# Performance work log

Measured on AMD Instinct MI355X. Metric: run time of the kernel, lower is better.

The kernel has to match this reference:

```python
import jax, jax.numpy as jnp
import numpy as np

N, L, H, D = 2, 4096, 12, 64
HD = H * D

def setup_inputs() -> dict:
    key = jax.random.key(0)
    ks = jax.random.split(key, 5)
    s = 1.0 / np.sqrt(HD)  # keep projections well-scaled
    return {
        "x": jax.random.normal(ks[0], (N, L, HD), dtype=jnp.float32),
        "Wq": jax.random.normal(ks[1], (HD, HD), dtype=jnp.float32) * s,
        "bq": jnp.zeros((HD,), dtype=jnp.float32),
        "Wk": jax.random.normal(ks[2], (HD, HD), dtype=jnp.float32) * s,
        "bk": jnp.zeros((HD,), dtype=jnp.float32),
        "Wv": jax.random.normal(ks[3], (HD, HD), dtype=jnp.float32) * s,
        "bv": jnp.zeros((HD,), dtype=jnp.float32),
        "Wo": jax.random.normal(ks[4], (HD, HD), dtype=jnp.float32) * s,
        "bo": jnp.zeros((HD,), dtype=jnp.float32),
        "train": 0,
    }

def reference(x, Wq, bq, Wk, bk, Wv, bv, Wo, bo, train):
    n, l, hd = x.shape
    h, d = H, D
    # QKV projections (hk.Linear: x @ W + b), reshape to (n, l, h, d)
    q = (x @ Wq + bq).reshape(n, l, h, d)
    k = (x @ Wk + bk).reshape(n, l, h, d)
    v = (x @ Wv + bv).reshape(n, l, h, d)
    # scores: (n, q, k, h), scaled by sqrt(key_size)
    qkt = jnp.einsum('nqhd,nkhd->nqkh', q, k) / jnp.sqrt(jnp.float32(d))
    attn = jax.nn.softmax(qkt, axis=2)
    # eval mode: dropout_rate is 0.0, so dropout is identity
    o = jnp.einsum('nqkh,nkhd->nqhd', attn, v).reshape(n, l, hd)
    return o @ Wo + bo
```

## Files before the change

kernel.cpp:

```cpp
#include <hip/hip_runtime.h>

#define NN 2
#define LL 4096
#define HH 12
#define DD 64
#define HD_ 768
#define M_TOT (NN * LL)
#define KVSTRIDE 262144

typedef __bf16 bf16_t;
typedef _Float16 f16_t;
typedef __bf16 bf16x8 __attribute__((ext_vector_type(8)));
typedef __bf16 bf16x4 __attribute__((ext_vector_type(4)));
typedef _Float16 f16x2 __attribute__((ext_vector_type(2)));
typedef _Float16 f16x4 __attribute__((ext_vector_type(4)));
typedef _Float16 f16x8 __attribute__((ext_vector_type(8)));
typedef float floatx4 __attribute__((ext_vector_type(4)));
typedef float floatx16 __attribute__((ext_vector_type(16)));

#define QSCALE 0.1803368801111f

__device__ __forceinline__ void async_load16(const void* g, void* l) {
    __builtin_amdgcn_global_load_lds(
        (const __attribute__((address_space(1))) unsigned int*)(g),
        (__attribute__((address_space(3))) unsigned int*)(l),
        16, 0, 0);
}

__device__ __forceinline__ f16x2 pkrtz(float a, float b) {
    return __builtin_bit_cast(f16x2, __builtin_amdgcn_cvt_pkrtz(a, b));
}

__device__ __forceinline__ f16x4 shflx32(f16x4 v) {
    int2 iv = __builtin_bit_cast(int2, v);
    iv.x = __shfl_xor(iv.x, 32);
    iv.y = __shfl_xor(iv.y, 32);
    return __builtin_bit_cast(f16x4, iv);
}

__global__ void cvt_kernel(const float* __restrict__ src, bf16_t* __restrict__ dst, int n4) {
    int i = blockIdx.x * blockDim.x + threadIdx.x;
    if (i < n4) {
        const float4 v = ((const float4*)src)[i];
        bf16_t* d = dst + (size_t)i * 4;
        d[0] = (bf16_t)v.x; d[1] = (bf16_t)v.y; d[2] = (bf16_t)v.z; d[3] = (bf16_t)v.w;
    }
}

struct WtArgs { const float* W[4]; bf16_t* Wt[4]; };
__global__ void cvt_wt_kernel(WtArgs a) {
    const int z = blockIdx.z;
    int id = blockIdx.x * 256 + threadIdx.x;
    int k = id / HD_;
    int n = id % HD_;
    a.Wt[z][(size_t)n * HD_ + k] = (bf16_t)a.W[z][id];
}

__device__ __forceinline__ void gemm_tile128(
    const bf16_t* __restrict__ A, const bf16_t* __restrict__ Bt,
    bf16_t* As, bf16_t* Bs, int m0, int n0, floatx4 (&acc)[4][4])
{
    const int tid  = threadIdx.x;
    const int w    = tid >> 6, lane = tid & 63;
    const int quad = lane >> 4, l16 = lane & 15;
    const int wm = w >> 1, wn = w & 1;
    const int rsub = lane >> 3;
    const int csub = (lane & 7) * 8;

    const bf16_t* aBase = A + (size_t)(m0 + w * 32 + rsub) * HD_ + csub;
    const bf16_t* bBase = Bt + (size_t)(n0 + w * 32 + rsub) * HD_ + csub;

    for (int kt = 0; kt < HD_; kt += 64) {
        __syncthreads();
        for (int i = 0; i < 4; ++i) {
            const int ar = w * 32 + i * 8;
            async_load16(aBase + (size_t)i * 8 * HD_ + kt, As + ar * 64 + lane * 8);
            async_load16(bBase + (size_t)i * 8 * HD_ + kt, Bs + ar * 64 + lane * 8);
        }
        __syncthreads();
        for (int ks = 0; ks < 2; ++ks) {
            bf16x8 af[4], bf[4];
            for (int mi = 0; mi < 4; ++mi)
                af[mi] = *(const bf16x8*)&As[(wm * 64 + mi * 16 + l16) * 64 + ks * 32 + quad * 8];
            for (int ni = 0; ni < 4; ++ni)
                bf[ni] = *(const bf16x8*)&Bs[(wn * 64 + ni * 16 + l16) * 64 + ks * 32 + quad * 8];
            for (int mi = 0; mi < 4; ++mi)
                for (int ni = 0; ni < 4; ++ni)
                    acc[mi][ni] = __builtin_amdgcn_mfma_f32_16x16x32_bf16(
                        af[mi], bf[ni], acc[mi][ni], 0, 0, 0);
        }
    }
}

struct QKVArgs {
    const bf16_t* Bt[3];
    const float* bias[3];
    void* out[3];
};
__global__ __launch_bounds__(256) void gemm_qkv_kernel(const bf16_t* __restrict__ A, QKVArgs p)
{
    __shared__ __align__(16) bf16_t As[128 * 64];
    __shared__ __align__(16) bf16_t Bs[128 * 64];
    const int z = blockIdx.z;
    const int m0 = blockIdx.y * 128, n0 = blockIdx.x * 128;

    floatx4 acc[4][4] = {};
    gemm_tile128(A, p.Bt[z], As, Bs, m0, n0, acc);

    const int tid  = threadIdx.x;
    const int lane = tid & 63;
    const int quad = lane >> 4, l16 = lane & 15;
    const int w    = tid >> 6;
    const int wm = w >> 1, wn = w & 1;
    const float scale = (z == 0) ? QSCALE : 1.0f;
    const float* bias = p.bias[z];

    for (int ni = 0; ni < 4; ++ni) {
        const int col = n0 + wn * 64 + ni * 16 + l16;
        const float bv = bias[col];
        const int h = col >> 6, d = col & 63;
        for (int mi = 0; mi < 4; ++mi) {
            for (int r = 0; r < 4; ++r) {
                const int row = m0 + wm * 64 + mi * 16 + quad * 4 + r;
                const float val = (acc[mi][ni][r] + bv) * scale;
                const int nn = row >> 12, l = row & 4095;
                const size_t nhb = (size_t)(nn * HH + h) * KVSTRIDE;
                if (z == 0) {
                    ((bf16_t*)p.out[0])[(((size_t)nn * HH + h) * LL + l) * DD + d] = (bf16_t)val;
                } else if (z == 1) {
                    size_t idx = nhb + (size_t)((l >> 5) * 4 + (d >> 4)) * 512
                               + ((l & 31) + 32 * ((d >> 3) & 1)) * 8 + (d & 7);
                    ((bf16_t*)p.out[1])[idx] = (bf16_t)val;
                } else {
                    size_t idx = nhb + (size_t)(((l >> 6) * 2 + (d >> 5)) * 4 + ((l >> 4) & 3)) * 512
                               + ((d & 31) + 32 * ((l >> 3) & 1)) * 8 + (l & 7);
                    ((f16_t*)p.out[2])[idx] = (f16_t)val;
                }
            }
        }
    }
}

__global__ __launch_bounds__(256) void gemm_o_kernel(
    const bf16_t* __restrict__ A, const bf16_t* __restrict__ Bt,
    const float* __restrict__ bias, float* __restrict__ Cout)
{
    __shared__ __align__(16) bf16_t As[128 * 64];
    __shared__ __align__(16) bf16_t Bs[128 * 64];
    const int m0 = blockIdx.y * 128, n0 = blockIdx.x * 128;

    floatx4 acc[4][4] = {};
    gemm_tile128(A, Bt, As, Bs, m0, n0, acc);

    const int tid  = threadIdx.x;
    const int lane = tid & 63;
    const int quad = lane >> 4, l16 = lane & 15;
    const int w    = tid >> 6;
    const int wm = w >> 1, wn = w & 1;

    for (int ni = 0; ni < 4; ++ni) {
        const int col = n0 + wn * 64 + ni * 16 + l16;
        const float bv = bias[col];
        for (int mi = 0; mi < 4; ++mi)
            for (int r = 0; r < 4; ++r) {
                const int row = m0 + wm * 64 + mi * 16 + quad * 4 + r;
                Cout[(size_t)row * HD_ + col] = acc[mi][ni][r] + bv;
            }
    }
}

__global__ __launch_bounds__(256) void attn_kernel(
    const bf16_t* __restrict__ qg, const bf16_t* __restrict__ kf,
    const f16_t* __restrict__ vf, bf16_t* __restrict__ og)
{
    __shared__ union {
        struct {
            bf16_t Ks[8 * 512];
            f16_t  Vs[8 * 512];
        } s;
        bf16_t OT[128 * 72];
    } u;

    const int tid = threadIdx.x;
    const int w = tid >> 6, lane = tid & 63;
    const int l32 = lane & 31, hi = lane >> 5;
    const int qt0 = blockIdx.x * 128;
    const int nh = blockIdx.y;
    const int nIdx = nh / HH, hIdx = nh % HH;

    bf16x8 qfrag[4];
    {
        const bf16_t* qp = qg + ((size_t)nh * LL + qt0 + w * 32 + l32) * DD + hi * 8;
        for (int s = 0; s < 4; ++s) qfrag[s] = *(const bf16x8*)(qp + s * 16);
    }

    const bf16_t* ksrc = kf + (size_t)nh * KVSTRIDE + (2 * w) * 512 + lane * 8;
    const f16_t*  vsrc = vf + (size_t)nh * KVSTRIDE + (2 * w) * 512 + lane * 8;
    bf16_t* kdst0 = &u.s.Ks[(2 * w) * 512 + lane * 8];
    bf16_t* kdst1 = &u.s.Ks[(2 * w + 1) * 512 + lane * 8];
    f16_t*  vdst0 = &u.s.Vs[(2 * w) * 512 + lane * 8];
    f16_t*  vdst1 = &u.s.Vs[(2 * w + 1) * 512 + lane * 8];

    floatx16 oacc[2] = {};
    float rs = 0.f;

    for (int t = 0; t < LL / 64; ++t) {
        __syncthreads();
        async_load16(ksrc, kdst0);
        async_load16(ksrc + 512, kdst1);
        async_load16(vsrc, vdst0);
        async_load16(vsrc + 512, vdst1);
        ksrc += 4096; vsrc += 4096;
        __syncthreads();

        for (int kvb = 0; kvb < 2; ++kvb) {
            floatx16 sacc = {};
            for (int s = 0; s < 4; ++s) {
                bf16x8 ak = *(const bf16x8*)&u.s.Ks[(kvb * 4 + s) * 512 + lane * 8];
                sacc = __builtin_amdgcn_mfma_f32_32x32x16_bf16(ak, qfrag[s], sacc, 0, 0, 0);
            }
            for (int sub = 0; sub < 2; ++sub) {
                float p[8];
                for (int i = 0; i < 8; ++i) {
                    p[i] = __builtin_amdgcn_exp2f(sacc[sub * 8 + i]);
                    rs += p[i];
                }
                f16x2 l01 = pkrtz(p[0], p[1]), l23 = pkrtz(p[2], p[3]);
                f16x2 h45 = pkrtz(p[4], p[5]), h67 = pkrtz(p[6], p[7]);
                f16x4 Lo = __builtin_shufflevector(l01, l23, 0, 1, 2, 3);
                f16x4 Hh = __builtin_shufflevector(h45, h67, 0, 1, 2, 3);
                f16x4 swL = shflx32(Lo);
                f16x4 swH = shflx32(Hh);
                f16x4 a03 = hi ? swH : Lo;
                f16x4 a47 = hi ? Hh : swL;
                f16x8 pf = __builtin_shufflevector(a03, a47, 0, 1, 2, 3, 4, 5, 6, 7);
                const int kstep = kvb * 2 + sub;
                for (int db = 0; db < 2; ++db) {
                    f16x8 av = *(const f16x8*)&u.s.Vs[(db * 4 + kstep) * 512 + lane * 8];
                    oacc[db] = __builtin_amdgcn_mfma_f32_32x32x16_f16(av, pf, oacc[db], 0, 0, 0);
                }
            }
        }
    }

    rs += __shfl_xor(rs, 32);
    const float rinv = __builtin_amdgcn_rcpf(rs);

    __syncthreads();
    for (int db = 0; db < 2; ++db)
        for (int g = 0; g < 4; ++g) {
            bf16x4 o4;
            for (int r = 0; r < 4; ++r)
                o4[r] = (bf16_t)(oacc[db][g * 4 + r] * rinv);
            *(bf16x4*)&u.OT[(w * 32 + l32) * 72 + db * 32 + hi * 4 + g * 8] = o4;
        }
    __syncthreads();

    const int q = tid >> 1, hf = tid & 1;
    const bf16_t* src = &u.OT[q * 72 + hf * 32];
    bf16x8 r0 = *(const bf16x8*)(src + 0);
    bf16x8 r1 = *(const bf16x8*)(src + 8);
    bf16x8 r2 = *(const bf16x8*)(src + 16);
    bf16x8 r3 = *(const bf16x8*)(src + 24);
    bf16_t* dst = og + ((size_t)nIdx * LL + qt0 + q) * HD_ + hIdx * 64 + hf * 32;
    *(bf16x8*)(dst + 0)  = r0;
    *(bf16x8*)(dst + 8)  = r1;
    *(bf16x8*)(dst + 16) = r2;
    *(bf16x8*)(dst + 24) = r3;
}

extern "C" void kernel_launch(void* const* d_in, const int* in_sizes, int n_in,
                              void* d_out, int out_size, void* d_ws, size_t ws_size,
                              hipStream_t stream) {
    const float* x  = (const float*)d_in[0];
    const float* Wq = (const float*)d_in[1];
    const float* bq = (const float*)d_in[2];
    const float* Wk = (const float*)d_in[3];
    const float* bk = (const float*)d_in[4];
    const float* Wv = (const float*)d_in[5];
    const float* bv = (const float*)d_in[6];
    const float* Wo = (const float*)d_in[7];
    const float* bo = (const float*)d_in[8];

    char* ws = (char*)d_ws;
    const size_t xbytes = (size_t)M_TOT * HD_ * 2;
    const size_t wbytes = (size_t)HD_ * HD_ * 2;

    bf16_t* xb  = (bf16_t*)ws; ws += xbytes;
    bf16_t* wqt = (bf16_t*)ws; ws += wbytes;
    bf16_t* wkt = (bf16_t*)ws; ws += wbytes;
    bf16_t* wvt = (bf16_t*)ws; ws += wbytes;
    bf16_t* wot = (bf16_t*)ws; ws += wbytes;
    bf16_t* qb  = (bf16_t*)ws; ws += xbytes;
    bf16_t* kfb = (bf16_t*)ws; ws += xbytes;
    f16_t*  vfb = (f16_t*)ws;  ws += xbytes;
    bf16_t* ob  = (bf16_t*)ws; ws += xbytes;

    cvt_kernel<<<(M_TOT * HD_ / 4 + 255) / 256, 256, 0, stream>>>(x, xb, M_TOT * HD_ / 4);

    WtArgs wa;
    wa.W[0] = Wq; wa.W[1] = Wk; wa.W[2] = Wv; wa.W[3] = Wo;
    wa.Wt[0] = wqt; wa.Wt[1] = wkt; wa.Wt[2] = wvt; wa.Wt[3] = wot;
    cvt_wt_kernel<<<dim3(HD_ * HD_ / 256, 1, 4), 256, 0, stream>>>(wa);

    QKVArgs qa;
    qa.Bt[0] = wqt; qa.Bt[1] = wkt; qa.Bt[2] = wvt;
    qa.bias[0] = bq; qa.bias[1] = bk; qa.bias[2] = bv;
    qa.out[0] = qb; qa.out[1] = kfb; qa.out[2] = vfb;
    gemm_qkv_kernel<<<dim3(HD_ / 128, M_TOT / 128, 3), 256, 0, stream>>>(xb, qa);

    attn_kernel<<<dim3(LL / 128, NN * HH), 256, 0, stream>>>(qb, kfb, vfb, ob);

    gemm_o_kernel<<<dim3(HD_ / 128, M_TOT / 128), 256, 0, stream>>>(ob, wot, bo, (float*)d_out);
}
```

Baseline: 339.1 us.

## Split attention KV across wave pairs, stage QKV epilogue in LDS, tile weight transpose

The attention kernel now processes 64 queries per block, and the two wave pairs each cover half of the key sequence. Their partial outputs and row sums are combined in LDS at the end, which doubles the grid and raises parallelism. The V layout is changed so the cross-lane shuffle of P fragments is no longer needed. The QKV GEMM epilogue writes tiles into shared memory in the target layouts and then stores them with coalesced 16-byte writes, and the weight transpose uses an LDS-tiled kernel. Together these reduce scattered global stores, at the cost of extra syncs and LDS traffic in the epilogues.

```diff
diff --git a/kernel.cpp b/kernel.cpp
--- a/kernel.cpp
+++ b/kernel.cpp
@@ -11,7 +11,6 @@
 typedef __bf16 bf16_t;
 typedef _Float16 f16_t;
 typedef __bf16 bf16x8 __attribute__((ext_vector_type(8)));
-typedef __bf16 bf16x4 __attribute__((ext_vector_type(4)));
 typedef _Float16 f16x2 __attribute__((ext_vector_type(2)));
 typedef _Float16 f16x4 __attribute__((ext_vector_type(4)));
 typedef _Float16 f16x8 __attribute__((ext_vector_type(8)));
@@ -29,13 +28,6 @@
 
 __device__ __forceinline__ f16x2 pkrtz(float a, float b) {
     return __builtin_bit_cast(f16x2, __builtin_amdgcn_cvt_pkrtz(a, b));
-}
-
-__device__ __forceinline__ f16x4 shflx32(f16x4 v) {
-    int2 iv = __builtin_bit_cast(int2, v);
-    iv.x = __shfl_xor(iv.x, 32);
-    iv.y = __shfl_xor(iv.y, 32);
-    return __builtin_bit_cast(f16x4, iv);
 }
 
 __global__ void cvt_kernel(const float* __restrict__ src, bf16_t* __restrict__ dst, int n4) {
@@ -48,12 +40,33 @@
 }
 
 struct WtArgs { const float* W[4]; bf16_t* Wt[4]; };
-__global__ void cvt_wt_kernel(WtArgs a) {
+__global__ __launch_bounds__(256) void cvt_wt_kernel(WtArgs a) {
+    __shared__ bf16_t T[64 * 65];
     const int z = blockIdx.z;
-    int id = blockIdx.x * 256 + threadIdx.x;
-    int k = id / HD_;
-    int n = id % HD_;
-    a.Wt[z][(size_t)n * HD_ + k] = (bf16_t)a.W[z][id];
+    const int k0 = blockIdx.y * 64, n0 = blockIdx.x * 64;
+    const int tid = threadIdx.x;
+    {
+        const int k = tid >> 2;
+        const int nc = (tid & 3) * 16;
+        const float* src = a.W[z] + (size_t)(k0 + k) * HD_ + n0 + nc;
+        for (int i = 0; i < 4; ++i) {
+            float4 v = *(const float4*)(src + i * 4);
+            T[(nc + i * 4 + 0) * 65 + k] = (bf16_t)v.x;
+            T[(nc + i * 4 + 1) * 65 + k] = (bf16_t)v.y;
+            T[(nc + i * 4 + 2) * 65 + k] = (bf16_t)v.z;
+            T[(nc + i * 4 + 3) * 65 + k] = (bf16_t)v.w;
+        }
+    }
+    __syncthreads();
+    {
+        const int n = tid >> 2;
+        const int kc = (tid & 3) * 16;
+        bf16_t* dst = a.Wt[z] + (size_t)(n0 + n) * HD_ + k0 + kc;
+        bf16x8 v0, v1;
+        for (int j = 0; j < 8; ++j) { v0[j] = T[n * 65 + kc + j]; v1[j] = T[n * 65 + kc + 8 + j]; }
+        *(bf16x8*)dst = v0;
+        *(bf16x8*)(dst + 8) = v1;
+    }
 }
 
 __device__ __forceinline__ void gemm_tile128(
@@ -99,13 +112,12 @@
 };
 __global__ __launch_bounds__(256) void gemm_qkv_kernel(const bf16_t* __restrict__ A, QKVArgs p)
 {
-    __shared__ __align__(16) bf16_t As[128 * 64];
-    __shared__ __align__(16) bf16_t Bs[128 * 64];
+    __shared__ __align__(16) bf16_t S[2 * 128 * 64];
     const int z = blockIdx.z;
     const int m0 = blockIdx.y * 128, n0 = blockIdx.x * 128;
 
     floatx4 acc[4][4] = {};
-    gemm_tile128(A, p.Bt[z], As, Bs, m0, n0, acc);
+    gemm_tile128(A, p.Bt[z], S, S + 8192, m0, n0, acc);
 
     const int tid  = threadIdx.x;
     const int lane = tid & 63;
@@ -115,29 +127,45 @@
     const float scale = (z == 0) ? QSCALE : 1.0f;
     const float* bias = p.bias[z];
 
+    __syncthreads();
     for (int ni = 0; ni < 4; ++ni) {
-        const int col = n0 + wn * 64 + ni * 16 + l16;
-        const float bv = bias[col];
-        const int h = col >> 6, d = col & 63;
+        const int dl = ni * 16 + l16;
+        const float bv = bias[n0 + wn * 64 + dl];
         for (int mi = 0; mi < 4; ++mi) {
             for (int r = 0; r < 4; ++r) {
-                const int row = m0 + wm * 64 + mi * 16 + quad * 4 + r;
+                const int ll = wm * 64 + mi * 16 + quad * 4 + r;
                 const float val = (acc[mi][ni][r] + bv) * scale;
-                const int nn = row >> 12, l = row & 4095;
-                const size_t nhb = (size_t)(nn * HH + h) * KVSTRIDE;
-                if (z == 0) {
-                    ((bf16_t*)p.out[0])[(((size_t)nn * HH + h) * LL + l) * DD + d] = (bf16_t)val;
-                } else if (z == 1) {
-                    size_t idx = nhb + (size_t)((l >> 5) * 4 + (d >> 4)) * 512
-                               + ((l & 31) + 32 * ((d >> 3) & 1)) * 8 + (d & 7);
-                    ((bf16_t*)p.out[1])[idx] = (bf16_t)val;
-                } else {
-                    size_t idx = nhb + (size_t)(((l >> 6) * 2 + (d >> 5)) * 4 + ((l >> 4) & 3)) * 512
-                               + ((d & 31) + 32 * ((l >> 3) & 1)) * 8 + (l & 7);
-                    ((f16_t*)p.out[2])[idx] = (f16_t)val;
-                }
+                int off;
+                if (z == 0)
+                    off = ll * 64 + dl;
+                else if (z == 1)
+                    off = ((ll >> 5) * 4 + (dl >> 4)) * 512
+                        + ((ll & 31) + 32 * ((dl >> 3) & 1)) * 8 + (dl & 7);
+                else
+                    off = (((ll >> 6) * 2 + (dl >> 5)) * 4 + ((ll >> 4) & 3)) * 512
+                        + ((dl & 31) + 32 * ((ll >> 2) & 1)) * 8
+                        + ((ll & 3) + 4 * ((ll >> 3) & 1));
+                if (z == 2) ((f16_t*)S)[wn * 8192 + off] = (f16_t)val;
+                else        S[wn * 8192 + off] = (bf16_t)val;
             }
         }
+    }
+    __syncthreads();
+
+    const int ht = tid >> 7, idx = tid & 127;
+    const int nn = m0 >> 12, l0 = m0 & 4095;
+    const int h = (n0 >> 6) + ht;
+    char* dstBase;
+    if (z == 0)
+        dstBase = (char*)p.out[0] + (((size_t)(nn * HH + h) * LL + l0) * 64) * 2;
+    else if (z == 1)
+        dstBase = (char*)p.out[1] + ((size_t)(nn * HH + h) * KVSTRIDE + (size_t)(l0 >> 5) * 2048) * 2;
+    else
+        dstBase = (char*)p.out[2] + ((size_t)(nn * HH + h) * KVSTRIDE + (size_t)(l0 >> 6) * 4096) * 2;
+    const bf16_t* srcB = S + ht * 8192;
+    for (int c = 0; c < 8; ++c) {
+        const int cc = (c + idx) & 7;
+        *(bf16x8*)(dstBase + (idx * 64 + cc * 8) * 2) = *(const bf16x8*)(srcB + idx * 64 + cc * 8);
     }
 }
 
@@ -169,54 +197,50 @@
     }
 }
 
-__global__ __launch_bounds__(256) void attn_kernel(
+__global__ __launch_bounds__(256, 5) void attn_kernel(
     const bf16_t* __restrict__ qg, const bf16_t* __restrict__ kf,
     const f16_t* __restrict__ vf, bf16_t* __restrict__ og)
 {
     __shared__ union {
-        struct {
-            bf16_t Ks[8 * 512];
-            f16_t  Vs[8 * 512];
-        } s;
-        bf16_t OT[128 * 72];
+        struct { bf16_t Ks[2 * 8 * 512]; f16_t Vs[2 * 8 * 512]; } s;
+        struct { float T[64 * 65]; float rsb[64]; } e;
     } u;
 
     const int tid = threadIdx.x;
     const int w = tid >> 6, lane = tid & 63;
     const int l32 = lane & 31, hi = lane >> 5;
-    const int qt0 = blockIdx.x * 128;
+    const int half = w >> 1, wp = w & 1;
+    const int qt0 = blockIdx.x * 64;
     const int nh = blockIdx.y;
     const int nIdx = nh / HH, hIdx = nh % HH;
 
     bf16x8 qfrag[4];
     {
-        const bf16_t* qp = qg + ((size_t)nh * LL + qt0 + w * 32 + l32) * DD + hi * 8;
+        const bf16_t* qp = qg + ((size_t)nh * LL + qt0 + wp * 32 + l32) * DD + hi * 8;
         for (int s = 0; s < 4; ++s) qfrag[s] = *(const bf16x8*)(qp + s * 16);
     }
 
-    const bf16_t* ksrc = kf + (size_t)nh * KVSTRIDE + (2 * w) * 512 + lane * 8;
-    const f16_t*  vsrc = vf + (size_t)nh * KVSTRIDE + (2 * w) * 512 + lane * 8;
-    bf16_t* kdst0 = &u.s.Ks[(2 * w) * 512 + lane * 8];
-    bf16_t* kdst1 = &u.s.Ks[(2 * w + 1) * 512 + lane * 8];
-    f16_t*  vdst0 = &u.s.Vs[(2 * w) * 512 + lane * 8];
-    f16_t*  vdst1 = &u.s.Vs[(2 * w + 1) * 512 + lane * 8];
+    const bf16_t* ksrc = kf + (size_t)nh * KVSTRIDE + (size_t)(half * 64 + wp) * 2048 + lane * 8;
+    const f16_t*  vsrc = vf + (size_t)nh * KVSTRIDE + (size_t)(half * 64 + wp) * 2048 + lane * 8;
+    bf16_t* kdst = &u.s.Ks[(half * 8 + wp * 4) * 512 + lane * 8];
+    f16_t*  vdst = &u.s.Vs[(half * 8 + wp * 4) * 512 + lane * 8];
 
     floatx16 oacc[2] = {};
     float rs = 0.f;
 
-    for (int t = 0; t < LL / 64; ++t) {
+    for (int t = 0; t < 32; ++t) {
         __syncthreads();
-        async_load16(ksrc, kdst0);
-        async_load16(ksrc + 512, kdst1);
-        async_load16(vsrc, vdst0);
-        async_load16(vsrc + 512, vdst1);
+        for (int c = 0; c < 4; ++c) {
+            async_load16(ksrc + c * 512, kdst + c * 512);
+            async_load16(vsrc + c * 512, vdst + c * 512);
+        }
         ksrc += 4096; vsrc += 4096;
         __syncthreads();
 
         for (int kvb = 0; kvb < 2; ++kvb) {
             floatx16 sacc = {};
             for (int s = 0; s < 4; ++s) {
-                bf16x8 ak = *(const bf16x8*)&u.s.Ks[(kvb * 4 + s) * 512 + lane * 8];
+                bf16x8 ak = *(const bf16x8*)&u.s.Ks[(half * 8 + kvb * 4 + s) * 512 + lane * 8];
                 sacc = __builtin_amdgcn_mfma_f32_32x32x16_bf16(ak, qfrag[s], sacc, 0, 0, 0);
             }
             for (int sub = 0; sub < 2; ++sub) {
@@ -225,18 +249,14 @@
                     p[i] = __builtin_amdgcn_exp2f(sacc[sub * 8 + i]);
                     rs += p[i];
                 }
-                f16x2 l01 = pkrtz(p[0], p[1]), l23 = pkrtz(p[2], p[3]);
-                f16x2 h45 = pkrtz(p[4], p[5]), h67 = pkrtz(p[6], p[7]);
-                f16x4 Lo = __builtin_shufflevector(l01, l23, 0, 1, 2, 3);
-                f16x4 Hh = __builtin_shufflevector(h45, h67, 0, 1, 2, 3);
-                f16x4 swL = shflx32(Lo);
-                f16x4 swH = shflx32(Hh);
-                f16x4 a03 = hi ? swH : Lo;
-                f16x4 a47 = hi ? Hh : swL;
-                f16x8 pf = __builtin_shufflevector(a03, a47, 0, 1, 2, 3, 4, 5, 6, 7);
+                f16x2 ab = pkrtz(p[0], p[1]), cd = pkrtz(p[2], p[3]);
+                f16x2 ef = pkrtz(p[4], p[5]), gh = pkrtz(p[6], p[7]);
+                f16x4 lo4 = __builtin_shufflevector(ab, cd, 0, 1, 2, 3);
+                f16x4 hi4 = __builtin_shufflevector(ef, gh, 0, 1, 2, 3);
+                f16x8 pf = __builtin_shufflevector(lo4, hi4, 0, 1, 2, 3, 4, 5, 6, 7);
                 const int kstep = kvb * 2 + sub;
                 for (int db = 0; db < 2; ++db) {
-                    f16x8 av = *(const f16x8*)&u.s.Vs[(db * 4 + kstep) * 512 + lane * 8];
+                    f16x8 av = *(const f16x8*)&u.s.Vs[(half * 8 + db * 4 + kstep) * 512 + lane * 8];
                     oacc[db] = __builtin_amdgcn_mfma_f32_32x32x16_f16(av, pf, oacc[db], 0, 0, 0);
                 }
             }
@@ -244,29 +264,36 @@
     }
 
     rs += __shfl_xor(rs, 32);
-    const float rinv = __builtin_amdgcn_rcpf(rs);
-
-    __syncthreads();
-    for (int db = 0; db < 2; ++db)
-        for (int g = 0; g < 4; ++g) {
-            bf16x4 o4;
-            for (int r = 0; r < 4; ++r)
-                o4[r] = (bf16_t)(oacc[db][g * 4 + r] * rinv);
-            *(bf16x4*)&u.OT[(w * 32 + l32) * 72 + db * 32 + hi * 4 + g * 8] = o4;
-        }
-    __syncthreads();
-
-    const int q = tid >> 1, hf = tid & 1;
-    const bf16_t* src = &u.OT[q * 72 + hf * 32];
-    bf16x8 r0 = *(const bf16x8*)(src + 0);
-    bf16x8 r1 = *(const bf16x8*)(src + 8);
-    bf16x8 r2 = *(const bf16x8*)(src + 16);
-    bf16x8 r3 = *(const bf16x8*)(src + 24);
-    bf16_t* dst = og + ((size_t)nIdx * LL + qt0 + q) * HD_ + hIdx * 64 + hf * 32;
-    *(bf16x8*)(dst + 0)  = r0;
-    *(bf16x8*)(dst + 8)  = r1;
-    *(bf16x8*)(dst + 16) = r2;
-    *(bf16x8*)(dst + 24) = r3;
+
+    const int q = wp * 32 + l32;
+    __syncthreads();
+    if (half == 0) {
+        for (int db = 0; db < 2; ++db)
+            for (int g = 0; g < 4; ++g)
+                for (int r = 0; r < 4; ++r)
+                    u.e.T[q * 65 + db * 32 + hi * 4 + g * 8 + r] = oacc[db][g * 4 + r];
+        if (lane < 32) u.e.rsb[q] = rs;
+    }
+    __syncthreads();
+    if (half == 1) {
+        for (int db = 0; db < 2; ++db)
+            for (int g = 0; g < 4; ++g)
+                for (int r = 0; r < 4; ++r)
+                    u.e.T[q * 65 + db * 32 + hi * 4 + g * 8 + r] += oacc[db][g * 4 + r];
+        if (lane < 32) u.e.rsb[q] += rs;
+    }
+    __syncthreads();
+
+    const int qo = tid >> 2, c = tid & 3;
+    const float rinv = __builtin_amdgcn_rcpf(u.e.rsb[qo]);
+    bf16x8 o0, o1;
+    for (int j = 0; j < 8; ++j) {
+        o0[j] = (bf16_t)(u.e.T[qo * 65 + c * 16 + j] * rinv);
+        o1[j] = (bf16_t)(u.e.T[qo * 65 + c * 16 + 8 + j] * rinv);
+    }
+    bf16_t* dst = og + ((size_t)nIdx * LL + qt0 + qo) * HD_ + hIdx * 64 + c * 16;
+    *(bf16x8*)dst = o0;
+    *(bf16x8*)(dst + 8) = o1;
 }
 
 extern "C" void kernel_launch(void* const* d_in, const int* in_sizes, int n_in,
@@ -301,7 +328,7 @@
     WtArgs wa;
     wa.W[0] = Wq; wa.W[1] = Wk; wa.W[2] = Wv; wa.W[3] = Wo;
     wa.Wt[0] = wqt; wa.Wt[1] = wkt; wa.Wt[2] = wvt; wa.Wt[3] = wot;
-    cvt_wt_kernel<<<dim3(HD_ * HD_ / 256, 1, 4), 256, 0, stream>>>(wa);
+    cvt_wt_kernel<<<dim3(12, 12, 4), 256, 0, stream>>>(wa);
 
     QKVArgs qa;
     qa.Bt[0] = wqt; qa.Bt[1] = wkt; qa.Bt[2] = wvt;
@@ -309,7 +336,7 @@
     qa.out[0] = qb; qa.out[1] = kfb; qa.out[2] = vfb;
     gemm_qkv_kernel<<<dim3(HD_ / 128, M_TOT / 128, 3), 256, 0, stream>>>(xb, qa);
 
-    attn_kernel<<<dim3(LL / 128, NN * HH), 256, 0, stream>>>(qb, kfb, vfb, ob);
+    attn_kernel<<<dim3(LL / 64, NN * HH), 256, 0, stream>>>(qb, kfb, vfb, ob);
 
     gemm_o_kernel<<<dim3(HD_ / 128, M_TOT / 128), 256, 0, stream>>>(ob, wot, bo, (float*)d_out);
 }
```

New measurement: 378.6 us. 11.6% more time.
